# Kernel optimization log

Hardware: AMD Instinct MI355X
Metric: run time of the kernel (lower is better)

## Reference

```python
import jax, jax.numpy as jnp
import numpy as np

N = 50000      # nodes
E = 800000     # edges (before self-loops)
F_IN = 256     # feature_size
H = 96         # hidden_channels
G = 64         # graphs in batch
NC = 4         # num_classes
EPS = 1e-5     # BatchNorm eps


def _lrelu(x, s=0.01):
    return jnp.where(x >= 0, x, s * x)


def _gat(x, W, a_s, a_d, b, src, dst):
    # PyG GATConv, heads=1: linear transform, edge-wise LeakyReLU(0.2) scores,
    # segment softmax over destination nodes, scatter-add aggregation.
    h = x @ W                                                  # [N,H]
    e = _lrelu((h * a_s).sum(-1)[src] + (h * a_d).sum(-1)[dst], 0.2)  # [E+N]
    m = jax.ops.segment_max(e, dst, num_segments=N)
    ee = jnp.exp(e - m[dst])
    denom = jax.ops.segment_sum(ee, dst, num_segments=N)
    alpha = ee / denom[dst]
    return jax.ops.segment_sum(alpha[:, None] * h[src], dst, num_segments=N) + b


def _bn(x, g, b):
    # training-mode BatchNorm over the node dimension
    mu = x.mean(0)
    var = ((x - mu) ** 2).mean(0)
    return g * (x - mu) / jnp.sqrt(var + EPS) + b


def setup_inputs() -> dict:
    key = jax.random.key(0)
    ks = jax.random.split(key, 20)
    p = lambda i, sh: jax.random.normal(ks[i], sh, jnp.float32) * 0.05
    inp = {
        "x": jax.random.normal(ks[0], (N, F_IN), jnp.float32),
        "edge_index": jax.random.randint(ks[1], (2, E), 0, N),
        "batch": jnp.sort(jax.random.randint(ks[2], (N,), 0, G)),
        "embed_W": p(3, (F_IN, H)), "embed_b": jnp.zeros((H,), jnp.float32),
        "conv1_W": p(4, (H, H)), "conv1_as": p(5, (H,)), "conv1_ad": p(6, (H,)), "conv1_b": jnp.zeros((H,), jnp.float32),
        "conv2_W": p(7, (H, H)), "conv2_as": p(8, (H,)), "conv2_ad": p(9, (H,)), "conv2_b": jnp.zeros((H,), jnp.float32),
        "conv3_W": p(10, (H, H)), "conv3_as": p(11, (H,)), "conv3_ad": p(12, (H,)), "conv3_b": jnp.zeros((H,), jnp.float32),
        "fc1_W": p(13, (H, H)), "fc1_b": jnp.zeros((H,), jnp.float32),
        "fc2_W": p(14, (H, H)), "fc2_b": jnp.zeros((H,), jnp.float32),
        "bn1_g": jnp.ones((H,), jnp.float32), "bn1_b": jnp.zeros((H,), jnp.float32),
        "bn2_g": jnp.ones((H,), jnp.float32), "bn2_b": jnp.zeros((H,), jnp.float32),
        "bn3_g": jnp.ones((H,), jnp.float32), "bn3_b": jnp.zeros((H,), jnp.float32),
        "fc3_W": p(15, (H, H // 2)), "fc3_b": jnp.zeros((H // 2,), jnp.float32),
        "fc4_W": p(16, (H // 2, NC)), "fc4_b": jnp.zeros((NC,), jnp.float32),
    }
    return inp


def reference(x, edge_index, batch, embed_W, embed_b,
              conv1_W, conv1_as, conv1_ad, conv1_b,
              conv2_W, conv2_as, conv2_ad, conv2_b,
              conv3_W, conv3_as, conv3_ad, conv3_b,
              fc1_W, fc1_b, fc2_W, fc2_b,
              bn1_g, bn1_b, bn2_g, bn2_b, bn3_g, bn3_b,
              fc3_W, fc3_b, fc4_W, fc4_b):
    loops = jnp.arange(N)
    src = jnp.concatenate([edge_index[0], loops])   # GATConv add_self_loops=True
    dst = jnp.concatenate([edge_index[1], loops])

    h = _lrelu(x @ embed_W + embed_b)
    identity = h
    h = _lrelu(_bn(_gat(h, conv1_W, conv1_as, conv1_ad, conv1_b, src, dst), bn1_g, bn1_b)) + identity
    h = _lrelu(h @ fc1_W + fc1_b)
    h = _lrelu(_bn(_gat(h, conv2_W, conv2_as, conv2_ad, conv2_b, src, dst), bn2_g, bn2_b)) + identity
    h = _lrelu(h @ fc2_W + fc2_b)
    h = _lrelu(_bn(_gat(h, conv3_W, conv3_as, conv3_ad, conv3_b, src, dst), bn3_g, bn3_b)) + identity

    # Poincare ball expmap0 with c=1: tanh(||u||) * u / ||u||
    n = jnp.maximum(jnp.linalg.norm(h, axis=-1, keepdims=True), 1e-15)
    h = jnp.tanh(n) * h / n

    cnt = jax.ops.segment_sum(jnp.ones((N,), h.dtype), batch, num_segments=G)
    pooled = jax.ops.segment_sum(h, batch, num_segments=G) / jnp.maximum(cnt, 1.0)[:, None]

    o = _lrelu(pooled @ fc3_W + fc3_b)
    return o @ fc4_W + fc4_b
```

## Files before the change

kernel.cpp:

```cpp
#include <hip/hip_runtime.h>
#include <hip/hip_bf16.h>

#define DEVINL __device__ __forceinline__

constexpr int N_NODES = 50000;
constexpr int N_EDGES = 800000;
constexpr int F_IN    = 256;
constexpr int H       = 96;
constexpr int NG      = 64;
constexpr float BN_EPS = 1e-5f;
constexpr int SLOT    = 64;
constexpr int NREP    = 8;
constexpr int REPSZ   = NG * H + NG;
constexpr int BNREP   = 64;

constexpr int NBLK1 = 160;
constexpr int EPT1  = N_EDGES / NBLK1;
constexpr int NBUCK = 196;
constexpr int BCAP  = 128;

typedef short bf16x8 __attribute__((ext_vector_type(8)));
typedef float f32x4  __attribute__((ext_vector_type(4)));
typedef unsigned int u32x4 __attribute__((ext_vector_type(4)));

DEVINL float bf2f(unsigned int u) {
    union { unsigned int i; float f; } c; c.i = u << 16; return c.f;
}
DEVINL unsigned short f2bf(float f) {
    union { float f; unsigned int i; } c; c.f = f;
    unsigned int x = c.i;
    return (unsigned short)((x + 0x7fffu + ((x >> 16) & 1u)) >> 16);
}
DEVINL float lrelu01(float v) { return v >= 0.f ? v : 0.01f * v; }
DEVINL float ldf(const void* p, size_t i, int f32) {
    return f32 ? ((const float*)p)[i] : bf2f(((const unsigned short*)p)[i]);
}
DEVINL u32x4 ntld4(const void* p) {
    return __builtin_nontemporal_load((const u32x4*)p);
}

__global__ __launch_bounds__(256) void setup_k(
    const unsigned short* __restrict__ x,
    int* __restrict__ flag,
    const void* __restrict__ sE, const void* __restrict__ s0,
    const void* __restrict__ s1, const void* __restrict__ s2,
    const void* __restrict__ s3, const void* __restrict__ s4,
    unsigned short* __restrict__ dE, unsigned short* __restrict__ d0,
    unsigned short* __restrict__ d1, unsigned short* __restrict__ d2,
    unsigned short* __restrict__ d3, unsigned short* __restrict__ d4)
{
    if (blockIdx.x == 0 && threadIdx.x < 64) {
        int l = threadIdx.x;
        float f = bf2f(x[l]);
        bool huge = !(fabsf(f) <= 1e4f);
        unsigned long long m = __ballot(huge);
        if (l == 0) flag[0] = (__popcll(m) >= 8) ? 1 : 0;
    }
    float ff = bf2f(x[threadIdx.x & 63]);
    bool huge = !(fabsf(ff) <= 1e4f);
    unsigned long long mm = __ballot(huge);
    int lf32 = (__popcll(mm) >= 8) ? 1 : 0;

    int bb = blockIdx.x;
    const void* src; unsigned short* dst; int K, i0;
    if (bb < 96) { src = sE; dst = dE; K = F_IN; i0 = bb * 256; }
    else {
        int m = (bb - 96) / 36, r = (bb - 96) % 36;
        K = H; i0 = r * 256;
        if      (m == 0) { src = s0; dst = d0; }
        else if (m == 1) { src = s1; dst = d1; }
        else if (m == 2) { src = s2; dst = d2; }
        else if (m == 3) { src = s3; dst = d3; }
        else             { src = s4; dst = d4; }
    }
    int i = i0 + threadIdx.x;
    if (i >= K * 96) return;
    int c   = i / 3072;
    int rem = i - c * 3072;
    int t    = rem >> 9;
    int rem2 = rem & 511;
    int l = rem2 >> 3, j = rem2 & 7;
    int k = c * 32 + (l >> 4) * 8 + j;
    int n = t * 16 + (l & 15);
    if (lf32) dst[i] = f2bf(((const float*)src)[k * 96 + n]);
    else      dst[i] = ((const unsigned short*)src)[k * 96 + n];
}

__global__ __launch_bounds__(256, 4) void embconv_k(
    const void* __restrict__ xp, const unsigned short* __restrict__ WpkE,
    const void* __restrict__ embB, const unsigned short* __restrict__ Wcv,
    const int* __restrict__ dflag,
    unsigned short* __restrict__ ident, unsigned short* __restrict__ out,
    const void* __restrict__ as_, const void* __restrict__ ad_,
    float* __restrict__ s, float* __restrict__ d,
    const int* __restrict__ ei, uint2* __restrict__ bbuf,
    int* __restrict__ bcnt,
    float* __restrict__ bnsumR, int M)
{
    __shared__ unsigned short R[64][104];
    __shared__ int lcur[NBUCK];

    {
        int zi = blockIdx.x * 256 + threadIdx.x;
        if (zi < BNREP * 192) bnsumR[zi] = 0.f;
    }

    if ((int)blockIdx.x < NBLK1) {
        for (int i = threadIdx.x; i < NBUCK; i += 256) lcur[i] = 0;
        __syncthreads();
        int base = (int)blockIdx.x * EPT1;
        int end  = base + EPT1;
        for (int e = base + (int)threadIdx.x; e < end; e += 256) {
            int sv = __builtin_nontemporal_load(ei + e);
            int dv = __builtin_nontemporal_load(ei + N_EDGES + e);
            int b  = dv >> 8;
            int pos = atomicAdd(&lcur[b], 1);
            if (pos < BCAP)
                bbuf[((size_t)blockIdx.x * NBUCK + b) * BCAP + pos] =
                    make_uint2((unsigned)sv, (unsigned)dv);
        }
        __syncthreads();
        for (int i = threadIdx.x; i < NBUCK; i += 256)
            bcnt[(int)blockIdx.x * NBUCK + i] = min(lcur[i], BCAP);
        return;
    }

    const int gb   = (int)blockIdx.x - NBLK1;
    const int f32  = dflag[0];
    const int l    = threadIdx.x & 63;
    const int wave = threadIdx.x >> 6;
    const int row0 = gb * 64 + wave * 16;
    const int m    = l & 15;
    const int q    = l >> 4;
    const int arow = row0 + m;
    const bool aok = arow < M;

    bf16x8 av[8];
    #pragma unroll
    for (int c = 0; c < 8; c++) {
        bf16x8 a = {};
        if (aok) {
            if (f32) {
                const float* A = (const float*)xp + (size_t)arow * F_IN + c * 32 + q * 8;
                u32x4 u0 = ntld4(A);
                u32x4 u1 = ntld4(A + 4);
                #pragma unroll
                for (int j = 0; j < 4; j++) a[j]     = (short)f2bf(__uint_as_float(u0[j]));
                #pragma unroll
                for (int j = 0; j < 4; j++) a[4 + j] = (short)f2bf(__uint_as_float(u1[j]));
            } else {
                union { u32x4 u; bf16x8 h; } cv;
                cv.u = ntld4((const unsigned short*)xp + (size_t)arow * F_IN + c * 32 + q * 8);
                a = cv.h;
            }
        }
        av[c] = a;
    }

    f32x4 acc[6] = {};
    const bf16x8* wp1 = (const bf16x8*)WpkE;
    #pragma unroll
    for (int c = 0; c < 8; c++) {
        const int base = c * 384 + l;
        #pragma unroll
        for (int t = 0; t < 6; t++)
            acc[t] = __builtin_amdgcn_mfma_f32_16x16x32_bf16(av[c], wp1[base + t * 64], acc[t], 0, 0, 0);
    }

    float bv[6];
    #pragma unroll
    for (int t = 0; t < 6; t++) bv[t] = ldf(embB, t * 16 + m, f32);
    #pragma unroll
    for (int r = 0; r < 4; r++) {
        int lr = wave * 16 + q * 4 + r;
        int rr = row0 + q * 4 + r;
        #pragma unroll
        for (int t = 0; t < 6; t++) {
            unsigned short sv = f2bf(lrelu01(acc[t][r] + bv[t]));
            R[lr][t * 16 + m] = sv;
            if (rr < M) ident[(size_t)rr * 96 + m + t * 16] = sv;
        }
    }
    __syncthreads();

    bf16x8 a2[3];
    #pragma unroll
    for (int c = 0; c < 3; c++)
        a2[c] = *(const bf16x8*)&R[wave * 16 + m][c * 32 + q * 8];

    f32x4 acc2[6] = {};
    const bf16x8* wp2 = (const bf16x8*)Wcv;
    #pragma unroll
    for (int c = 0; c < 3; c++) {
        const int base = c * 384 + l;
        #pragma unroll
        for (int t = 0; t < 6; t++)
            acc2[t] = __builtin_amdgcn_mfma_f32_16x16x32_bf16(a2[c], wp2[base + t * 64], acc2[t], 0, 0, 0);
    }

    #pragma unroll
    for (int r = 0; r < 4; r++) {
        int rr = row0 + q * 4 + r;
        if (rr >= M) continue;
        size_t o = (size_t)rr * 96 + m;
        #pragma unroll
        for (int t = 0; t < 6; t++)
            out[o + t * 16] = f2bf(acc2[t][r]);
    }

    float asv[6], adv[6];
    #pragma unroll
    for (int t = 0; t < 6; t++) {
        asv[t] = ldf(as_, t * 16 + m, f32);
        adv[t] = ldf(ad_, t * 16 + m, f32);
    }
    #pragma unroll
    for (int r = 0; r < 4; r++) {
        float ps = 0.f, pd = 0.f;
        #pragma unroll
        for (int t = 0; t < 6; t++) {
            ps = fmaf(acc2[t][r], asv[t], ps);
            pd = fmaf(acc2[t][r], adv[t], pd);
        }
        #pragma unroll
        for (int off = 1; off < 16; off <<= 1) {
            ps += __shfl_xor(ps, off);
            pd += __shfl_xor(pd, off);
        }
        int rr = row0 + q * 4 + r;
        if (m == 0 && rr < M) { s[rr] = ps; d[rr] = pd; }
    }
}

__global__ __launch_bounds__(256) void csr_k(
    const uint2* __restrict__ bbuf, const int* __restrict__ bcnt,
    unsigned short* __restrict__ col, int* __restrict__ fill)
{
    __shared__ unsigned short slots[256][SLOT];
    __shared__ int lcnt[256];
    __shared__ int ccnt[NBLK1];

    int b = blockIdx.x, tid = threadIdx.x;
    lcnt[tid] = 0;
    for (int i = tid; i < NBLK1; i += 256) ccnt[i] = bcnt[i * NBUCK + b];
    __syncthreads();

    int n0 = b << 8;
    for (int g = tid; g < NBLK1 * BCAP; g += 256) {
        int blk = g >> 7;
        int i   = g & (BCAP - 1);
        if (i < ccnt[blk]) {
            uint2 e = bbuf[((size_t)blk * NBUCK + b) * BCAP + i];
            int local = (int)e.y - n0;
            int slot = atomicAdd(&lcnt[local], 1);
            if (slot < SLOT) slots[local][slot] = (unsigned short)e.x;
        }
    }
    __syncthreads();

    const uint4* ls = (const uint4*)slots;
    for (int i = tid; i < 256 * 8; i += 256) {
        int node = n0 + (i >> 3);
        if (node < N_NODES)
            ((uint4*)col)[(size_t)node * 8 + (i & 7)] = ls[i];
    }
    int node = n0 + tid;
    if (node < N_NODES) fill[node] = lcnt[tid];
}

__global__ __launch_bounds__(256, 4) void fcconv_k(
    const unsigned short* __restrict__ Ap,
    const unsigned short* __restrict__ Wfc, const void* __restrict__ bfc,
    const unsigned short* __restrict__ Wcv,
    const int* __restrict__ dflag,
    unsigned short* __restrict__ out,
    const void* __restrict__ as_, const void* __restrict__ ad_,
    float* __restrict__ s, float* __restrict__ d,
    const float* __restrict__ coefp, const unsigned short* __restrict__ idn,
    float* __restrict__ bnsumR, int M)
{
    __shared__ unsigned short R[64][104];

    {
        int zi = blockIdx.x * 256 + threadIdx.x;
        if (zi < BNREP * 192) bnsumR[zi] = 0.f;
    }

    const int wf32 = dflag[0];
    const int l    = threadIdx.x & 63;
    const int wave = threadIdx.x >> 6;
    const int row0 = blockIdx.x * 64 + wave * 16;
    const int m    = l & 15;
    const int q    = l >> 4;
    const int arow = row0 + m;
    const bool aok = arow < M;

    bf16x8 av[3];
    #pragma unroll
    for (int c = 0; c < 3; c++) {
        bf16x8 a = {};
        if (aok) {
            const int f0 = c * 32 + q * 8;
            uint4 xu = *(const uint4*)(Ap  + (size_t)arow * H + f0);
            uint4 iu = *(const uint4*)(idn + (size_t)arow * H + f0);
            unsigned int xs[4] = { xu.x, xu.y, xu.z, xu.w };
            unsigned int is[4] = { iu.x, iu.y, iu.z, iu.w };
            #pragma unroll
            for (int jj = 0; jj < 4; jj++) {
                int f = f0 + 2 * jj;
                float v0 = lrelu01(bf2f(xs[jj] & 0xffff) * coefp[f]     + coefp[96 + f])     + bf2f(is[jj] & 0xffff);
                float v1 = lrelu01(bf2f(xs[jj] >> 16)    * coefp[f + 1] + coefp[96 + f + 1]) + bf2f(is[jj] >> 16);
                a[2 * jj]     = (short)f2bf(v0);
                a[2 * jj + 1] = (short)f2bf(v1);
            }
        }
        av[c] = a;
    }

    f32x4 acc[6] = {};
    const bf16x8* wp1 = (const bf16x8*)Wfc;
    #pragma unroll
    for (int c = 0; c < 3; c++) {
        const int base = c * 384 + l;
        #pragma unroll
        for (int t = 0; t < 6; t++)
            acc[t] = __builtin_amdgcn_mfma_f32_16x16x32_bf16(av[c], wp1[base + t * 64], acc[t], 0, 0, 0);
    }

    float bv[6];
    #pragma unroll
    for (int t = 0; t < 6; t++) bv[t] = ldf(bfc, t * 16 + m, wf32);
    #pragma unroll
    for (int r = 0; r < 4; r++) {
        int lr = wave * 16 + q * 4 + r;
        #pragma unroll
        for (int t = 0; t < 6; t++)
            R[lr][t * 16 + m] = f2bf(lrelu01(acc[t][r] + bv[t]));
    }
    __syncthreads();

    bf16x8 a2[3];
    #pragma unroll
    for (int c = 0; c < 3; c++)
        a2[c] = *(const bf16x8*)&R[wave * 16 + m][c * 32 + q * 8];

    f32x4 acc2[6] = {};
    const bf16x8* wp2 = (const bf16x8*)Wcv;
    #pragma unroll
    for (int c = 0; c < 3; c++) {
        const int base = c * 384 + l;
        #pragma unroll
        for (int t = 0; t < 6; t++)
            acc2[t] = __builtin_amdgcn_mfma_f32_16x16x32_bf16(a2[c], wp2[base + t * 64], acc2[t], 0, 0, 0);
    }

    #pragma unroll
    for (int r = 0; r < 4; r++) {
        int rr = row0 + q * 4 + r;
        if (rr >= M) continue;
        size_t o = (size_t)rr * 96 + m;
        #pragma unroll
        for (int t = 0; t < 6; t++)
            out[o + t * 16] = f2bf(acc2[t][r]);
    }

    float asv[6], adv[6];
    #pragma unroll
    for (int t = 0; t < 6; t++) {
        asv[t] = ldf(as_, t * 16 + m, wf32);
        adv[t] = ldf(ad_, t * 16 + m, wf32);
    }
    #pragma unroll
    for (int r = 0; r < 4; r++) {
        float ps = 0.f, pd = 0.f;
        #pragma unroll
        for (int t = 0; t < 6; t++) {
            ps = fmaf(acc2[t][r], asv[t], ps);
            pd = fmaf(acc2[t][r], adv[t], pd);
        }
        #pragma unroll
        for (int off = 1; off < 16; off <<= 1) {
            ps += __shfl_xor(ps, off);
            pd += __shfl_xor(pd, off);
        }
        int rr = row0 + q * 4 + r;
        if (m == 0 && rr < M) { s[rr] = ps; d[rr] = pd; }
    }
}

__global__ __launch_bounds__(256) void agg_k(
    const unsigned short* __restrict__ h2, const float* __restrict__ s,
    const float* __restrict__ d, const int* __restrict__ fill,
    const unsigned short* __restrict__ col, const void* __restrict__ bias,
    const int* __restrict__ dflag, unsigned short* __restrict__ out,
    float* __restrict__ bnsumR, float* __restrict__ zp, int M)
{
    __shared__ uint2 uwb[4][80];
    __shared__ float lstat[4][192];
    if (zp) {
        int zi = blockIdx.x * 256 + threadIdx.x;
        if (zi < NREP * REPSZ) zp[zi] = 0.f;
    }
    int f32 = dflag[0];
    int v = (blockIdx.x * blockDim.x + threadIdx.x) >> 6;
    int l = threadIdx.x & 63;
    int wv = threadIdx.x >> 6;
    bool act = v < M;
    bool hw = (l < 48);
    int  c2 = 2 * l;
    float o0 = 0.f, o1 = 0.f;

    if (act) {
        int st   = v * SLOT;
        int degr = min(fill[v], SLOT - 1);
        int deg  = degr + 1;

        float dv = d[v];
        int u = 0; float e = -1e30f;
        if (l < degr) {
            u = col[st + l];
            float t = s[u] + dv;
            e = t >= 0.f ? t : 0.2f * t;
        } else if (l == degr) {
            u = v;
            float t = s[v] + dv;
            e = t >= 0.f ? t : 0.2f * t;
        }
        float lm = e;
        #pragma unroll
        for (int off = 32; off > 0; off >>= 1) lm = fmaxf(lm, __shfl_xor(lm, off));
        float w = (l < deg) ? __expf(e - lm) : 0.f;
        float lsum = w;
        #pragma unroll
        for (int off = 32; off > 0; off >>= 1) lsum += __shfl_xor(lsum, off);
        float rden = 1.0f / lsum;

        uwb[wv][l] = make_uint2((unsigned int)u, __float_as_uint(w));
        if (l < 16) uwb[wv][64 + l] = make_uint2(0u, 0u);

        float a0 = 0.f, a1 = 0.f;
        const uint2* myuw = uwb[wv];
        for (int j = 0; j < deg; j += 16) {
            int lim = deg - j;
            uint2 p[16];
            #pragma unroll
            for (int k = 0; k < 16; k++) p[k] = myuw[j + k];
            if (hw) {
                unsigned int hv[16];
                #pragma unroll
                for (int k = 0; k < 16; k++)
                    hv[k] = (k < lim) ? *(const unsigned int*)(h2 + (size_t)p[k].x * 96 + c2) : 0u;
                #pragma unroll
                for (int k = 0; k < 16; k++) {
                    float wj = __uint_as_float(p[k].y);
                    a0 = fmaf(wj, bf2f(hv[k] & 0xffff), a0);
                    a1 = fmaf(wj, bf2f(hv[k] >> 16),    a1);
                }
            }
        }
        if (hw) {
            float b0 = ldf(bias, c2,     f32);
            float b1 = ldf(bias, c2 + 1, f32);
            unsigned int o = (unsigned int)f2bf(a0 * rden + b0)
                           | ((unsigned int)f2bf(a1 * rden + b1) << 16);
            *(unsigned int*)(out + (size_t)v * 96 + c2) = o;
            o0 = bf2f(o & 0xffff);
            o1 = bf2f(o >> 16);
        }
    }

    if (hw) {
        lstat[wv][c2]          = o0;
        lstat[wv][c2 + 1]      = o1;
        lstat[wv][96 + c2]     = o0 * o0;
        lstat[wv][97 + c2]     = o1 * o1;
    }
    __syncthreads();
    if (threadIdx.x < 192) {
        float tot = lstat[0][threadIdx.x] + lstat[1][threadIdx.x]
                  + lstat[2][threadIdx.x] + lstat[3][threadIdx.x];
        atomicAdd(&bnsumR[(blockIdx.x & (BNREP - 1)) * 192 + threadIdx.x], tot);
    }
}

__global__ void bncoef_k(const float* __restrict__ bnsumR,
                         const void* __restrict__ g_,
                         const void* __restrict__ b_,
                         const int* __restrict__ dflag,
                         float* __restrict__ coef)
{
    __shared__ float tot[192];
    int t = threadIdx.x;
    if (t < 192) {
        float s = 0.f;
        #pragma unroll 8
        for (int r = 0; r < BNREP; r++) s += bnsumR[r * 192 + t];
        tot[t] = s;
    }
    __syncthreads();
    if (t < 96) {
        int f32 = dflag[0];
        float mu  = tot[t] * (1.f / N_NODES);
        float var = tot[96 + t] * (1.f / N_NODES) - mu * mu;
        float rinv = 1.0f / sqrtf(var + BN_EPS);
        float sc = ldf(g_, t, f32) * rinv;
        coef[t]      = sc;
        coef[96 + t] = ldf(b_, t, f32) - mu * sc;
    }
}

__global__ __launch_bounds__(256) void bnpool_k(
    const unsigned short* __restrict__ h, const float* __restrict__ coef,
    const unsigned short* __restrict__ iden, const int* __restrict__ batch,
    float* __restrict__ pooled8, int M)
{
    int w = (blockIdx.x * blockDim.x + threadIdx.x) >> 6;
    int l = threadIdx.x & 63;
    int v0 = w * 16;
    if (v0 >= M) return;
    float* P = pooled8 + (blockIdx.x & (NREP - 1)) * REPSZ;
    float* C = P + NG * H;
    bool hw = (l < 48);
    int  c2 = 2 * l;
    float sc0 = 0.f, sc1 = 0.f, sh0 = 0.f, sh1 = 0.f;
    if (hw) {
        sc0 = coef[c2]; sc1 = coef[c2 + 1];
        sh0 = coef[96 + c2]; sh1 = coef[97 + c2];
    }
    int nv = min(16, M - v0);

    int gb[16];
    #pragma unroll
    for (int k = 0; k < 16; k++) gb[k] = batch[v0 + min(k, nv - 1)];

    float x0[16], x1[16], q[16];
    #pragma unroll
    for (int k = 0; k < 16; k++) { x0[k] = 0.f; x1[k] = 0.f; q[k] = 0.f; }
    if (hw) {
        unsigned int xu[16], iu[16];
        #pragma unroll
        for (int k = 0; k < 16; k++) {
            int v = v0 + k;
            if (k < nv) {
                xu[k] = *(const unsigned int*)(h    + (size_t)v * 96 + c2);
                iu[k] = *(const unsigned int*)(iden + (size_t)v * 96 + c2);
            } else { xu[k] = 0u; iu[k] = 0u; }
        }
        #pragma unroll
        for (int k = 0; k < 16; k++) {
            x0[k] = lrelu01(bf2f(xu[k] & 0xffff) * sc0 + sh0) + bf2f(iu[k] & 0xffff);
            x1[k] = lrelu01(bf2f(xu[k] >> 16)    * sc1 + sh1) + bf2f(iu[k] >> 16);
            q[k]  = x0[k] * x0[k] + x1[k] * x1[k];
        }
    }

    #pragma unroll
    for (int off = 32; off > 0; off >>= 1) {
        #pragma unroll
        for (int k = 0; k < 16; k++) q[k] += __shfl_xor(q[k], off);
    }

    float f[16];
    #pragma unroll
    for (int k = 0; k < 16; k++) {
        float n = fmaxf(sqrtf(q[k]), 1e-15f);
        if (n < 15.f) {
            float t = __expf(2.f * n);
            f[k] = (t - 1.f) / ((t + 1.f) * n);
        } else {
            f[k] = 1.f / n;
        }
    }

    float a0 = 0.f, a1 = 0.f, cnt = 0.f;
    int curg = -1;
    for (int k = 0; k < nv; k++) {
        int g = gb[k];
        if (g != curg) {
            if (curg >= 0) {
                if (hw) {
                    atomicAdd(&P[curg * 96 + c2],     a0);
                    atomicAdd(&P[curg * 96 + c2 + 1], a1);
                }
                if (l == 0) atomicAdd(&C[curg], cnt);
            }
            a0 = a1 = 0.f; cnt = 0.f; curg = g;
        }
        a0 = fmaf(f[k], x0[k], a0);
        a1 = fmaf(f[k], x1[k], a1);
        cnt += 1.f;
    }
    if (curg >= 0) {
        if (hw) {
            atomicAdd(&P[curg * 96 + c2],     a0);
            atomicAdd(&P[curg * 96 + c2 + 1], a1);
        }
        if (l == 0) atomicAdd(&C[curg], cnt);
    }
}

__global__ __launch_bounds__(64) void head_k(const float* __restrict__ pooled8,
                                             const void* __restrict__ w3,
                                             const void* __restrict__ b3,
                                             const void* __restrict__ w4,
                                             const void* __restrict__ b4,
                                             const int* __restrict__ dflag,
                                             void* __restrict__ outv)
{
    int g = blockIdx.x;
    int t = threadIdx.x;
    int f32 = dflag[0];
    __shared__ float p[96];
    __shared__ float o[48];
    float cs = 0.f;
    #pragma unroll
    for (int r = 0; r < NREP; r++) cs += pooled8[r * REPSZ + NG * H + g];
    float inv = 1.0f / fmaxf(cs, 1.0f);
    for (int c = t; c < 96; c += 64) {
        float v = 0.f;
        #pragma unroll
        for (int r = 0; r < NREP; r++) v += pooled8[r * REPSZ + g * 96 + c];
        p[c] = v * inv;
    }
    __syncthreads();
    if (t < 48) {
        float a = ldf(b3, t, f32);
        #pragma unroll
        for (int c = 0; c < 96; c++) a = fmaf(p[c], ldf(w3, (size_t)c * 48 + t, f32), a);
        o[t] = lrelu01(a);
    }
    __syncthreads();
    if (t < 4) {
        float a = ldf(b4, t, f32);
        #pragma unroll
        for (int j = 0; j < 48; j++) a = fmaf(o[j], ldf(w4, j * 4 + t, f32), a);
        if (f32) ((float*)outv)[g * 4 + t] = a;
        else     ((unsigned short*)outv)[g * 4 + t] = f2bf(a);
    }
}

extern "C" void kernel_launch(void* const* d_in, const int* in_sizes, int n_in,
                              void* d_out, int out_size, void* d_ws, size_t ws_size,
                              hipStream_t stream)
{
    const void* x     = d_in[0];
    const int*  ei    = (const int*)d_in[1];
    const int*  batch = (const int*)d_in[2];
    const void* embW  = d_in[3];
    const void* embB  = d_in[4];
    const void* convW[3]  = { d_in[5],  d_in[9],  d_in[13] };
    const void* convAs[3] = { d_in[6],  d_in[10], d_in[14] };
    const void* convAd[3] = { d_in[7],  d_in[11], d_in[15] };
    const void* convB[3]  = { d_in[8],  d_in[12], d_in[16] };
    const void* fcW[2]    = { d_in[17], d_in[19] };
    const void* fcB[2]    = { d_in[18], d_in[20] };
    const void* bnG[3]    = { d_in[21], d_in[23], d_in[25] };
    const void* bnB[3]    = { d_in[22], d_in[24], d_in[26] };
    const void* fc3W = d_in[27];
    const void* fc3b = d_in[28];
    const void* fc4W = d_in[29];
    const void* fc4b = d_in[30];

    char* wp_ = (char*)d_ws;
    auto alloc = [&](size_t b) { char* p = wp_; wp_ += (b + 255) & ~(size_t)255; return p; };
    int*   dflag = (int*)alloc(256);
    unsigned short* ident = (unsigned short*)alloc((size_t)N_NODES * H * 2);
    unsigned short* hA    = (unsigned short*)alloc((size_t)N_NODES * H * 2);
    unsigned short* hB    = (unsigned short*)alloc((size_t)N_NODES * H * 2);
    float* s_sc  = (float*)alloc((size_t)N_NODES * 4);
    float* d_sc  = (float*)alloc((size_t)N_NODES * 4);
    float* bnsumR = (float*)alloc((size_t)BNREP * 192 * 4);
    float* coef  = (float*)alloc(192 * 4);
    float* pooled8 = (float*)alloc((size_t)NREP * REPSZ * 4);
    int*   fill  = (int*)alloc((size_t)N_NODES * 4);
    unsigned short* col = (unsigned short*)alloc((size_t)N_NODES * SLOT * 2);
    uint2* bbuf = (uint2*)alloc((size_t)NBLK1 * NBUCK * BCAP * 8);
    int*   bcnt = (int*)alloc((size_t)NBLK1 * NBUCK * 4);
    unsigned short* wpkEmb = (unsigned short*)alloc((size_t)F_IN * 96 * 2);
    unsigned short* wpkS[5];
    for (int i = 0; i < 5; i++) wpkS[i] = (unsigned short*)alloc((size_t)H * 96 * 2);

    const int GM = (N_NODES + 63) / 64;
    const int GW = (N_NODES * 64 + 255) / 256;
    const int GP = ((N_NODES + 15) / 16 * 64 + 255) / 256;

    setup_k<<<276, 256, 0, stream>>>(
        (const unsigned short*)x, dflag,
        embW, convW[0], convW[1], convW[2], fcW[0], fcW[1],
        wpkEmb, wpkS[0], wpkS[1], wpkS[2], wpkS[3], wpkS[4]);

    embconv_k<<<NBLK1 + GM, 256, 0, stream>>>(
        x, wpkEmb, embB, wpkS[0], dflag, ident, hB,
        convAs[0], convAd[0], s_sc, d_sc,
        ei, bbuf, bcnt, bnsumR, N_NODES);

    csr_k<<<NBUCK, 256, 0, stream>>>(bbuf, bcnt, col, fill);

    agg_k<<<GW, 256, 0, stream>>>(hB, s_sc, d_sc, fill, col, convB[0], dflag, hA,
                                  bnsumR, nullptr, N_NODES);
    bncoef_k<<<1, 192, 0, stream>>>(bnsumR, bnG[0], bnB[0], dflag, coef);
    fcconv_k<<<GM, 256, 0, stream>>>(hA, wpkS[3], fcB[0], wpkS[1], dflag, hB,
                                     convAs[1], convAd[1], s_sc, d_sc,
                                     coef, ident, bnsumR, N_NODES);

    agg_k<<<GW, 256, 0, stream>>>(hB, s_sc, d_sc, fill, col, convB[1], dflag, hA,
                                  bnsumR, nullptr, N_NODES);
    bncoef_k<<<1, 192, 0, stream>>>(bnsumR, bnG[1], bnB[1], dflag, coef);
    fcconv_k<<<GM, 256, 0, stream>>>(hA, wpkS[4], fcB[1], wpkS[2], dflag, hB,
                                     convAs[2], convAd[2], s_sc, d_sc,
                                     coef, ident, bnsumR, N_NODES);

    agg_k<<<GW, 256, 0, stream>>>(hB, s_sc, d_sc, fill, col, convB[2], dflag, hA,
                                  bnsumR, pooled8, N_NODES);
    bncoef_k<<<1, 192, 0, stream>>>(bnsumR, bnG[2], bnB[2], dflag, coef);

    bnpool_k<<<GP, 256, 0, stream>>>(hA, coef, ident, batch, pooled8, N_NODES);
    head_k<<<NG, 64, 0, stream>>>(pooled8, fc3W, fc3b, fc4W, fc4b, dflag, d_out);
}
```

Baseline: 370.7 us.

## Shift edge bucketing into setup kernel and CSR build into embedding kernel

Moves the edge-bucketing phase into the weight-packing setup kernel as extra blocks, and moves the CSR slot-building phase into the embedding/conv kernel as extra blocks that run alongside the GEMM blocks. This removes one kernel launch and lets the graph-construction work overlap with the dense work. Buckets shrink to 128 nodes (391 buckets, cap 64 per block-bucket) so the CSR stage fits in a shared-memory union with the GEMM tile. The smaller per-bucket capacity makes overflow truncation more likely, but the expected load of about 16 edges per block-bucket leaves ample headroom.

Result: faster. 356.7 us (-3.8%).

```diff
diff --git a/kernel.cpp b/kernel.cpp
--- a/kernel.cpp
+++ b/kernel.cpp
@@ -16,8 +16,9 @@
 
 constexpr int NBLK1 = 160;
 constexpr int EPT1  = N_EDGES / NBLK1;
-constexpr int NBUCK = 196;
-constexpr int BCAP  = 128;
+constexpr int NBUCK = 391;
+constexpr int BCAP  = 64;
+constexpr int NPACK = 276;
 
 typedef short bf16x8 __attribute__((ext_vector_type(8)));
 typedef float f32x4  __attribute__((ext_vector_type(4)));
@@ -42,6 +43,8 @@
 __global__ __launch_bounds__(256) void setup_k(
     const unsigned short* __restrict__ x,
     int* __restrict__ flag,
+    const int* __restrict__ ei, uint2* __restrict__ bbuf,
+    int* __restrict__ bcnt,
     const void* __restrict__ sE, const void* __restrict__ s0,
     const void* __restrict__ s1, const void* __restrict__ s2,
     const void* __restrict__ s3, const void* __restrict__ s4,
@@ -49,6 +52,29 @@
     unsigned short* __restrict__ d1, unsigned short* __restrict__ d2,
     unsigned short* __restrict__ d3, unsigned short* __restrict__ d4)
 {
+    __shared__ int lcur[NBUCK];
+
+    if ((int)blockIdx.x >= NPACK) {
+        int blk = (int)blockIdx.x - NPACK;
+        for (int i = threadIdx.x; i < NBUCK; i += 256) lcur[i] = 0;
+        __syncthreads();
+        int base = blk * EPT1;
+        int end  = base + EPT1;
+        for (int e = base + (int)threadIdx.x; e < end; e += 256) {
+            int sv = __builtin_nontemporal_load(ei + e);
+            int dv = __builtin_nontemporal_load(ei + N_EDGES + e);
+            int b  = dv >> 7;
+            int pos = atomicAdd(&lcur[b], 1);
+            if (pos < BCAP)
+                bbuf[((size_t)blk * NBUCK + b) * BCAP + pos] =
+                    make_uint2((unsigned)sv, (unsigned)dv);
+        }
+        __syncthreads();
+        for (int i = threadIdx.x; i < NBUCK; i += 256)
+            bcnt[blk * NBUCK + i] = min(lcur[i], BCAP);
+        return;
+    }
+
     if (blockIdx.x == 0 && threadIdx.x < 64) {
         int l = threadIdx.x;
         float f = bf2f(x[l]);
@@ -93,39 +119,58 @@
     unsigned short* __restrict__ ident, unsigned short* __restrict__ out,
     const void* __restrict__ as_, const void* __restrict__ ad_,
     float* __restrict__ s, float* __restrict__ d,
-    const int* __restrict__ ei, uint2* __restrict__ bbuf,
-    int* __restrict__ bcnt,
+    const uint2* __restrict__ bbuf, const int* __restrict__ bcnt,
+    unsigned short* __restrict__ col, int* __restrict__ fill,
     float* __restrict__ bnsumR, int M)
 {
-    __shared__ unsigned short R[64][104];
-    __shared__ int lcur[NBUCK];
+    union SMem {
+        struct {
+            unsigned short slots[128][SLOT];
+            int lcnt[128];
+            int ccnt[NBLK1];
+        } c;
+        unsigned short R[64][104];
+    };
+    __shared__ SMem sm;
 
     {
         int zi = blockIdx.x * 256 + threadIdx.x;
         if (zi < BNREP * 192) bnsumR[zi] = 0.f;
     }
 
-    if ((int)blockIdx.x < NBLK1) {
-        for (int i = threadIdx.x; i < NBUCK; i += 256) lcur[i] = 0;
+    if ((int)blockIdx.x < NBUCK) {
+        int b = blockIdx.x, tid = threadIdx.x;
+        if (tid < 128) sm.c.lcnt[tid] = 0;
+        for (int i = tid; i < NBLK1; i += 256) sm.c.ccnt[i] = bcnt[i * NBUCK + b];
         __syncthreads();
-        int base = (int)blockIdx.x * EPT1;
-        int end  = base + EPT1;
-        for (int e = base + (int)threadIdx.x; e < end; e += 256) {
-            int sv = __builtin_nontemporal_load(ei + e);
-            int dv = __builtin_nontemporal_load(ei + N_EDGES + e);
-            int b  = dv >> 8;
-            int pos = atomicAdd(&lcur[b], 1);
-            if (pos < BCAP)
-                bbuf[((size_t)blockIdx.x * NBUCK + b) * BCAP + pos] =
-                    make_uint2((unsigned)sv, (unsigned)dv);
+
+        int n0 = b << 7;
+        for (int g = tid; g < NBLK1 * BCAP; g += 256) {
+            int blk = g >> 6;
+            int i   = g & (BCAP - 1);
+            if (i < sm.c.ccnt[blk]) {
+                uint2 e = bbuf[((size_t)blk * NBUCK + b) * BCAP + i];
+                int local = (int)e.y - n0;
+                int slot = atomicAdd(&sm.c.lcnt[local], 1);
+                if (slot < SLOT) sm.c.slots[local][slot] = (unsigned short)e.x;
+            }
         }
         __syncthreads();
-        for (int i = threadIdx.x; i < NBUCK; i += 256)
-            bcnt[(int)blockIdx.x * NBUCK + i] = min(lcur[i], BCAP);
+
+        const uint4* ls = (const uint4*)sm.c.slots;
+        for (int i = tid; i < 128 * 8; i += 256) {
+            int node = n0 + (i >> 3);
+            if (node < N_NODES)
+                ((uint4*)col)[(size_t)node * 8 + (i & 7)] = ls[i];
+        }
+        if (tid < 128) {
+            int node = n0 + tid;
+            if (node < N_NODES) fill[node] = sm.c.lcnt[tid];
+        }
         return;
     }
 
-    const int gb   = (int)blockIdx.x - NBLK1;
+    const int gb   = (int)blockIdx.x - NBUCK;
     const int f32  = dflag[0];
     const int l    = threadIdx.x & 63;
     const int wave = threadIdx.x >> 6;
@@ -177,7 +222,7 @@
         #pragma unroll
         for (int t = 0; t < 6; t++) {
             unsigned short sv = f2bf(lrelu01(acc[t][r] + bv[t]));
-            R[lr][t * 16 + m] = sv;
+            sm.R[lr][t * 16 + m] = sv;
             if (rr < M) ident[(size_t)rr * 96 + m + t * 16] = sv;
         }
     }
@@ -186,7 +231,7 @@
     bf16x8 a2[3];
     #pragma unroll
     for (int c = 0; c < 3; c++)
-        a2[c] = *(const bf16x8*)&R[wave * 16 + m][c * 32 + q * 8];
+        a2[c] = *(const bf16x8*)&sm.R[wave * 16 + m][c * 32 + q * 8];
 
     f32x4 acc2[6] = {};
     const bf16x8* wp2 = (const bf16x8*)Wcv;
@@ -230,42 +275,6 @@
         int rr = row0 + q * 4 + r;
         if (m == 0 && rr < M) { s[rr] = ps; d[rr] = pd; }
     }
-}
-
-__global__ __launch_bounds__(256) void csr_k(
-    const uint2* __restrict__ bbuf, const int* __restrict__ bcnt,
-    unsigned short* __restrict__ col, int* __restrict__ fill)
-{
-    __shared__ unsigned short slots[256][SLOT];
-    __shared__ int lcnt[256];
-    __shared__ int ccnt[NBLK1];
-
-    int b = blockIdx.x, tid = threadIdx.x;
-    lcnt[tid] = 0;
-    for (int i = tid; i < NBLK1; i += 256) ccnt[i] = bcnt[i * NBUCK + b];
-    __syncthreads();
-
-    int n0 = b << 8;
-    for (int g = tid; g < NBLK1 * BCAP; g += 256) {
-        int blk = g >> 7;
-        int i   = g & (BCAP - 1);
-        if (i < ccnt[blk]) {
-            uint2 e = bbuf[((size_t)blk * NBUCK + b) * BCAP + i];
-            int local = (int)e.y - n0;
-            int slot = atomicAdd(&lcnt[local], 1);
-            if (slot < SLOT) slots[local][slot] = (unsigned short)e.x;
-        }
-    }
-    __syncthreads();
-
-    const uint4* ls = (const uint4*)slots;
-    for (int i = tid; i < 256 * 8; i += 256) {
-        int node = n0 + (i >> 3);
-        if (node < N_NODES)
-            ((uint4*)col)[(size_t)node * 8 + (i & 7)] = ls[i];
-    }
-    int node = n0 + tid;
-    if (node < N_NODES) fill[node] = lcnt[tid];
 }
 
 __global__ __launch_bounds__(256, 4) void fcconv_k(
@@ -684,17 +693,16 @@
     const int GW = (N_NODES * 64 + 255) / 256;
     const int GP = ((N_NODES + 15) / 16 * 64 + 255) / 256;
 
-    setup_k<<<276, 256, 0, stream>>>(
+    setup_k<<<NPACK + NBLK1, 256, 0, stream>>>(
         (const unsigned short*)x, dflag,
+        ei, bbuf, bcnt,
         embW, convW[0], convW[1], convW[2], fcW[0], fcW[1],
         wpkEmb, wpkS[0], wpkS[1], wpkS[2], wpkS[3], wpkS[4]);
 
-    embconv_k<<<NBLK1 + GM, 256, 0, stream>>>(
+    embconv_k<<<NBUCK + GM, 256, 0, stream>>>(
         x, wpkEmb, embB, wpkS[0], dflag, ident, hB,
         convAs[0], convAd[0], s_sc, d_sc,
-        ei, bbuf, bcnt, bnsumR, N_NODES);
-
-    csr_k<<<NBUCK, 256, 0, stream>>>(bbuf, bcnt, col, fill);
+        bbuf, bcnt, col, fill, bnsumR, N_NODES);
 
     agg_k<<<GW, 256, 0, stream>>>(hB, s_sc, d_sc, fill, col, convB[0], dflag, hA,
                                   bnsumR, nullptr, N_NODES);
```
